# Kernel tuning notes

Measured on AMD Instinct MI355X. Metric: run time of the kernel, lower is better.

The kernel has to match this reference:

```python
import jax, jax.numpy as jnp
import numpy as np


def setup_inputs() -> dict:
    key = jax.random.key(0)
    k1, k2, k3 = jax.random.split(key, 3)
    B, H, D, N = 2, 16, 64, 2048
    return {
        "query": jax.random.normal(k1, (B, H, D, N), dtype=jnp.float32),
        "key": jax.random.normal(k2, (B, H, D, N), dtype=jnp.float32),
        "value": jax.random.normal(k3, (B, H, D, N), dtype=jnp.float32),
    }


def reference(query, key, value):
    # NOTE: original torch code scales by sqrt(query.size(-1)) which,
    # given the [B,H,d,N] layout, is sqrt(N) (the sequence length), not sqrt(d).
    scale = query.shape[-1] ** 0.5
    # scores[b,h,q,k] = sum_d query[b,h,d,q] * key[b,h,d,k]
    scores = jnp.einsum("bhdq,bhdk->bhqk", query, key) / scale
    attn = jax.nn.softmax(scores, axis=-1)
    # out[b,h,q,v] = sum_k attn[b,h,q,k] * value[b,h,v,k]
    return jnp.einsum("bhqk,bhvk->bhqv", attn, value)
```

## Files before the change

### kernel.cpp

```cpp
#include <hip/hip_runtime.h>
#include <hip/hip_bf16.h>


typedef __attribute__((ext_vector_type(8))) short short8;
typedef __attribute__((ext_vector_type(4))) float f32x4;

#define NN 2048
#define DD 64
#define ROWB 144

#if __has_builtin(__builtin_amdgcn_exp2f)
#define EXP2(x) __builtin_amdgcn_exp2f(x)
#else
#define EXP2(x) __expf(0.69314718056f * (x))
#endif

__device__ __forceinline__ unsigned pk2(float a, float b) {
  __hip_bfloat162 h = __float22bfloat162_rn(make_float2(a, b));
  unsigned u; __builtin_memcpy(&u, &h, 4); return u;
}
__device__ __forceinline__ short f2bf(float f) {
  union { float f; unsigned u; } x; x.f = f;
  unsigned r = (x.u + 0x7fffu + ((x.u >> 16) & 1u)) >> 16;
  return (short)r;
}

__global__ __launch_bounds__(256, 2) void attn_kernel(
    const float* __restrict__ Q, const float* __restrict__ K,
    const float* __restrict__ V, float* __restrict__ Out) {
  const int tid  = threadIdx.x;
  const int wave = tid >> 6, lane = tid & 63;
  const int quad = lane >> 4, l16 = lane & 15;

  const int bh   = blockIdx.x >> 4;
  const int qblk = blockIdx.x & 15;

  const float* Qh = Q + (size_t)bh * DD * NN;
  const float* Kh = K + (size_t)bh * DD * NN;
  const float* Vh = V + (size_t)bh * DD * NN;
  float*       Oh = Out + (size_t)bh * NN * DD;

  __shared__ __align__(16) char ldsK[2][64 * ROWB];
  __shared__ __align__(16) char ldsV[2][64 * ROWB];
  __shared__ __align__(16) char ldsP[8][16 * ROWB];

  const float qscale = 0.031881407f;
  short8 bQ[2][2];
  int qb[2];
#pragma unroll
  for (int qt = 0; qt < 2; ++qt) {
    qb[qt] = qblk * 128 + (wave * 2 + qt) * 16;
#pragma unroll
    for (int h = 0; h < 2; ++h)
#pragma unroll
      for (int j = 0; j < 8; ++j) {
        int d = h * 32 + quad * 8 + j;
        bQ[qt][h][j] = f2bf(Qh[(size_t)d * NN + qb[qt] + l16] * qscale);
      }
  }

  f32x4 accO[2][4];
#pragma unroll
  for (int qt = 0; qt < 2; ++qt)
#pragma unroll
    for (int vt = 0; vt < 4; ++vt) accO[qt][vt] = (f32x4){0.f, 0.f, 0.f, 0.f};
  float lp[2] = {0.f, 0.f};

  const int ka = tid & 31, kg = tid >> 5;
  const int vv = tid >> 2, vko = (tid & 3) * 16;
  const float* kbase0 = Kh + (size_t)(2 * ka) * NN + kg * 8;
  const float* kbase1 = kbase0 + NN;
  const float* vbase  = Vh + (size_t)vv * NN + vko;
  char* Pq0 = ldsP[wave * 2];
  char* Pq1 = ldsP[wave * 2 + 1];
  const int swr = l16 >> 1;

  float kA[8], kB[8], vA[16];
  auto load_kv = [&](int k0) {
    const float4* p0 = (const float4*)(kbase0 + k0);
    const float4* p1 = (const float4*)(kbase1 + k0);
    float4 a0 = p0[0], a1 = p0[1];
    float4 b0 = p1[0], b1 = p1[1];
    kA[0] = a0.x; kA[1] = a0.y; kA[2] = a0.z; kA[3] = a0.w;
    kA[4] = a1.x; kA[5] = a1.y; kA[6] = a1.z; kA[7] = a1.w;
    kB[0] = b0.x; kB[1] = b0.y; kB[2] = b0.z; kB[3] = b0.w;
    kB[4] = b1.x; kB[5] = b1.y; kB[6] = b1.z; kB[7] = b1.w;
    const float4* pv = (const float4*)(vbase + k0);
    float4 c0 = pv[0], c1 = pv[1], c2 = pv[2], c3 = pv[3];
    vA[0]  = c0.x; vA[1]  = c0.y; vA[2]  = c0.z; vA[3]  = c0.w;
    vA[4]  = c1.x; vA[5]  = c1.y; vA[6]  = c1.z; vA[7]  = c1.w;
    vA[8]  = c2.x; vA[9]  = c2.y; vA[10] = c2.z; vA[11] = c2.w;
    vA[12] = c3.x; vA[13] = c3.y; vA[14] = c3.z; vA[15] = c3.w;
  };
  auto store_kv = [&](char* bK, char* bV) {
#pragma unroll
    for (int j = 0; j < 8; ++j) {
      int k = kg * 8 + j;
      int grp = (ka >> 2) ^ ((k >> 1) & 7);
      *(unsigned*)&bK[k * ROWB + grp * 16 + (ka & 3) * 4] = pk2(kA[j], kB[j]);
    }
    uint4 w0 = make_uint4(pk2(vA[0], vA[1]),  pk2(vA[2], vA[3]),
                          pk2(vA[4], vA[5]),  pk2(vA[6], vA[7]));
    uint4 w1 = make_uint4(pk2(vA[8], vA[9]),  pk2(vA[10], vA[11]),
                          pk2(vA[12], vA[13]), pk2(vA[14], vA[15]));
    *(uint4*)&bV[vv * ROWB + vko * 2]      = w0;
    *(uint4*)&bV[vv * ROWB + vko * 2 + 16] = w1;
  };

  load_kv(0);
  store_kv(ldsK[0], ldsV[0]);
  __syncthreads();

  for (int it = 0; it < 32; ++it) {
    const int cur = it & 1;
    load_kv(((it + 1) & 31) * 64);

    const char* cK = ldsK[cur];
    const char* cV = ldsV[cur];

    f32x4 s[2][4];
#pragma unroll
    for (int kt = 0; kt < 4; ++kt) {
      const int key = kt * 16 + l16;
      short8 aK0 = *(const short8*)&cK[key * ROWB + ((quad) ^ swr) * 16];
      short8 aK1 = *(const short8*)&cK[key * ROWB + ((4 + quad) ^ swr) * 16];
      f32x4 z = (f32x4){0.f, 0.f, 0.f, 0.f};
      s[0][kt] = __builtin_amdgcn_mfma_f32_16x16x32_bf16(aK0, bQ[0][0], z, 0, 0, 0);
      s[0][kt] = __builtin_amdgcn_mfma_f32_16x16x32_bf16(aK1, bQ[0][1], s[0][kt], 0, 0, 0);
      s[1][kt] = __builtin_amdgcn_mfma_f32_16x16x32_bf16(aK0, bQ[1][0], z, 0, 0, 0);
      s[1][kt] = __builtin_amdgcn_mfma_f32_16x16x32_bf16(aK1, bQ[1][1], s[1][kt], 0, 0, 0);
    }

#pragma unroll
    for (int qt = 0; qt < 2; ++qt) {
      char* Pq = qt ? Pq1 : Pq0;
#pragma unroll
      for (int kt = 0; kt < 4; ++kt) {
        float p0 = EXP2(s[qt][kt][0]);
        float p1 = EXP2(s[qt][kt][1]);
        float p2 = EXP2(s[qt][kt][2]);
        float p3 = EXP2(s[qt][kt][3]);
        lp[qt] += (p0 + p1) + (p2 + p3);
        uint2 w; w.x = pk2(p0, p1); w.y = pk2(p2, p3);
        *(uint2*)&Pq[l16 * ROWB + kt * 32 + quad * 8] = w;
      }
    }

#pragma unroll
    for (int h2 = 0; h2 < 2; ++h2) {
      short8 aP0 = *(const short8*)&Pq0[l16 * ROWB + h2 * 64 + quad * 16];
      short8 aP1 = *(const short8*)&Pq1[l16 * ROWB + h2 * 64 + quad * 16];
#pragma unroll
      for (int vt = 0; vt < 4; ++vt) {
        short8 bV = *(const short8*)&cV[(vt * 16 + l16) * ROWB + h2 * 64 + quad * 16];
        accO[0][vt] = __builtin_amdgcn_mfma_f32_16x16x32_bf16(aP0, bV, accO[0][vt], 0, 0, 0);
        accO[1][vt] = __builtin_amdgcn_mfma_f32_16x16x32_bf16(aP1, bV, accO[1][vt], 0, 0, 0);
      }
    }

    store_kv(ldsK[cur ^ 1], ldsV[cur ^ 1]);
    __syncthreads();
  }

#pragma unroll
  for (int qt = 0; qt < 2; ++qt) {
    float l = lp[qt];
    l += __shfl_xor(l, 16, 64);
    l += __shfl_xor(l, 32, 64);
#pragma unroll
    for (int r = 0; r < 4; ++r) {
      float lr  = __shfl(l, quad * 4 + r, 64);
      float inv = 1.0f / lr;
      int q = qb[qt] + quad * 4 + r;
#pragma unroll
      for (int vt = 0; vt < 4; ++vt)
        Oh[(size_t)q * DD + vt * 16 + l16] = accO[qt][vt][r] * inv;
    }
  }
}

extern "C" void kernel_launch(void* const* d_in, const int* in_sizes, int n_in,
                              void* d_out, int out_size, void* d_ws, size_t ws_size,
                              hipStream_t stream) {
  const float* Q = (const float*)d_in[0];
  const float* K = (const float*)d_in[1];
  const float* V = (const float*)d_in[2];
  float* O = (float*)d_out;
  dim3 grid(2 * 16 * (NN / 128));
  attn_kernel<<<grid, dim3(256), 0, stream>>>(Q, K, V, O);
}
```

Baseline: 139.3 us.

## Switch to 32x32x16 MFMA and keep P in registers via permlane32 swap

Replaces the 16x16x32 MFMA tiling with 32x32x16 MFMAs, so each wave computes a 32-query by 64-key score tile as S^T. The exponentiated P values are packed to bf16 and rearranged across lane halves with v_permlane32_swap instead of being written to and re-read from a per-wave LDS buffer. This removes the P LDS round trip and its shared memory, and lowers instruction count per FLOP. In exchange it uses larger accumulator register sets, which may pressure occupancy, and relies on a gfx950-specific instruction.

```diff
diff --git a/kernel.cpp b/kernel.cpp
--- a/kernel.cpp
+++ b/kernel.cpp
@@ -3,7 +3,7 @@
 
 
 typedef __attribute__((ext_vector_type(8))) short short8;
-typedef __attribute__((ext_vector_type(4))) float f32x4;
+typedef __attribute__((ext_vector_type(16))) float f32x16;
 
 #define NN 2048
 #define DD 64
@@ -16,13 +16,16 @@
 #endif
 
 __device__ __forceinline__ unsigned pk2(float a, float b) {
-  __hip_bfloat162 h = __float22bfloat162_rn(make_float2(a, b));
-  unsigned u; __builtin_memcpy(&u, &h, 4); return u;
+  __hip_bfloat162 hh = __float22bfloat162_rn(make_float2(a, b));
+  unsigned u; __builtin_memcpy(&u, &hh, 4); return u;
 }
 __device__ __forceinline__ short f2bf(float f) {
   union { float f; unsigned u; } x; x.f = f;
   unsigned r = (x.u + 0x7fffu + ((x.u >> 16) & 1u)) >> 16;
   return (short)r;
+}
+__device__ __forceinline__ void pl32swap(unsigned &x, unsigned &y) {
+  asm("v_permlane32_swap_b32 %0, %1" : "+v"(x), "+v"(y));
 }
 
 __global__ __launch_bounds__(256, 2) void attn_kernel(
@@ -30,7 +33,7 @@
     const float* __restrict__ V, float* __restrict__ Out) {
   const int tid  = threadIdx.x;
   const int wave = tid >> 6, lane = tid & 63;
-  const int quad = lane >> 4, l16 = lane & 15;
+  const int m = lane & 31, h = lane >> 5;
 
   const int bh   = blockIdx.x >> 4;
   const int qblk = blockIdx.x & 15;
@@ -42,38 +45,30 @@
 
   __shared__ __align__(16) char ldsK[2][64 * ROWB];
   __shared__ __align__(16) char ldsV[2][64 * ROWB];
-  __shared__ __align__(16) char ldsP[8][16 * ROWB];
 
   const float qscale = 0.031881407f;
-  short8 bQ[2][2];
-  int qb[2];
+  const int qb = qblk * 128 + wave * 32;
+  short8 bQ[4];
 #pragma unroll
-  for (int qt = 0; qt < 2; ++qt) {
-    qb[qt] = qblk * 128 + (wave * 2 + qt) * 16;
+  for (int st = 0; st < 4; ++st)
 #pragma unroll
-    for (int h = 0; h < 2; ++h)
+    for (int j = 0; j < 8; ++j) {
+      int d = st * 16 + h * 8 + j;
+      bQ[st][j] = f2bf(Qh[(size_t)d * NN + qb + m] * qscale);
+    }
+
+  f32x16 accO[2];
 #pragma unroll
-      for (int j = 0; j < 8; ++j) {
-        int d = h * 32 + quad * 8 + j;
-        bQ[qt][h][j] = f2bf(Qh[(size_t)d * NN + qb[qt] + l16] * qscale);
-      }
-  }
-
-  f32x4 accO[2][4];
+  for (int vt = 0; vt < 2; ++vt)
 #pragma unroll
-  for (int qt = 0; qt < 2; ++qt)
-#pragma unroll
-    for (int vt = 0; vt < 4; ++vt) accO[qt][vt] = (f32x4){0.f, 0.f, 0.f, 0.f};
-  float lp[2] = {0.f, 0.f};
+    for (int i = 0; i < 16; ++i) accO[vt][i] = 0.f;
+  float lp = 0.f;
 
   const int ka = tid & 31, kg = tid >> 5;
   const int vv = tid >> 2, vko = (tid & 3) * 16;
   const float* kbase0 = Kh + (size_t)(2 * ka) * NN + kg * 8;
   const float* kbase1 = kbase0 + NN;
   const float* vbase  = Vh + (size_t)vv * NN + vko;
-  char* Pq0 = ldsP[wave * 2];
-  char* Pq1 = ldsP[wave * 2 + 1];
-  const int swr = l16 >> 1;
 
   float kA[8], kB[8], vA[16];
   auto load_kv = [&](int k0) {
@@ -111,6 +106,8 @@
   store_kv(ldsK[0], ldsV[0]);
   __syncthreads();
 
+  const int sw = (m >> 1) & 7;
+
   for (int it = 0; it < 32; ++it) {
     const int cur = it & 1;
     load_kv(((it + 1) & 31) * 64);
@@ -118,43 +115,50 @@
     const char* cK = ldsK[cur];
     const char* cV = ldsV[cur];
 
-    f32x4 s[2][4];
+    f32x16 sT0, sT1;
 #pragma unroll
-    for (int kt = 0; kt < 4; ++kt) {
-      const int key = kt * 16 + l16;
-      short8 aK0 = *(const short8*)&cK[key * ROWB + ((quad) ^ swr) * 16];
-      short8 aK1 = *(const short8*)&cK[key * ROWB + ((4 + quad) ^ swr) * 16];
-      f32x4 z = (f32x4){0.f, 0.f, 0.f, 0.f};
-      s[0][kt] = __builtin_amdgcn_mfma_f32_16x16x32_bf16(aK0, bQ[0][0], z, 0, 0, 0);
-      s[0][kt] = __builtin_amdgcn_mfma_f32_16x16x32_bf16(aK1, bQ[0][1], s[0][kt], 0, 0, 0);
-      s[1][kt] = __builtin_amdgcn_mfma_f32_16x16x32_bf16(aK0, bQ[1][0], z, 0, 0, 0);
-      s[1][kt] = __builtin_amdgcn_mfma_f32_16x16x32_bf16(aK1, bQ[1][1], s[1][kt], 0, 0, 0);
+    for (int i = 0; i < 16; ++i) { sT0[i] = 0.f; sT1[i] = 0.f; }
+#pragma unroll
+    for (int st = 0; st < 4; ++st) {
+      const int off = (((st * 2 + h) ^ sw) * 16);
+      short8 aK0 = *(const short8*)&cK[m * ROWB + off];
+      short8 aK1 = *(const short8*)&cK[(32 + m) * ROWB + off];
+      sT0 = __builtin_amdgcn_mfma_f32_32x32x16_bf16(aK0, bQ[st], sT0, 0, 0, 0);
+      sT1 = __builtin_amdgcn_mfma_f32_32x32x16_bf16(aK1, bQ[st], sT1, 0, 0, 0);
+    }
+
+    float p[2][16];
+#pragma unroll
+    for (int r = 0; r < 16; ++r) { p[0][r] = EXP2(sT0[r]); p[1][r] = EXP2(sT1[r]); }
+
+    unsigned u[2][4][2];
+#pragma unroll
+    for (int kt = 0; kt < 2; ++kt) {
+#pragma unroll
+      for (int g = 0; g < 4; ++g) {
+        u[kt][g][0] = pk2(p[kt][4 * g + 0], p[kt][4 * g + 1]);
+        u[kt][g][1] = pk2(p[kt][4 * g + 2], p[kt][4 * g + 3]);
+      }
+      float s0 = (p[kt][0]  + p[kt][1])  + (p[kt][2]  + p[kt][3]);
+      float s1 = (p[kt][4]  + p[kt][5])  + (p[kt][6]  + p[kt][7]);
+      float s2 = (p[kt][8]  + p[kt][9])  + (p[kt][10] + p[kt][11]);
+      float s3 = (p[kt][12] + p[kt][13]) + (p[kt][14] + p[kt][15]);
+      lp += (s0 + s1) + (s2 + s3);
     }
 
 #pragma unroll
-    for (int qt = 0; qt < 2; ++qt) {
-      char* Pq = qt ? Pq1 : Pq0;
+    for (int s = 0; s < 4; ++s) {
+      const int kt = s >> 1, ge = 2 * (s & 1);
+      unsigned t0 = u[kt][ge][0], t1 = u[kt][ge][1];
+      unsigned t2 = u[kt][ge + 1][0], t3 = u[kt][ge + 1][1];
+      pl32swap(t0, t2);
+      pl32swap(t1, t3);
+      short8 aP;
+      { unsigned w[4] = {t0, t1, t2, t3}; __builtin_memcpy(&aP, w, 16); }
 #pragma unroll
-      for (int kt = 0; kt < 4; ++kt) {
-        float p0 = EXP2(s[qt][kt][0]);
-        float p1 = EXP2(s[qt][kt][1]);
-        float p2 = EXP2(s[qt][kt][2]);
-        float p3 = EXP2(s[qt][kt][3]);
-        lp[qt] += (p0 + p1) + (p2 + p3);
-        uint2 w; w.x = pk2(p0, p1); w.y = pk2(p2, p3);
-        *(uint2*)&Pq[l16 * ROWB + kt * 32 + quad * 8] = w;
-      }
-    }
-
-#pragma unroll
-    for (int h2 = 0; h2 < 2; ++h2) {
-      short8 aP0 = *(const short8*)&Pq0[l16 * ROWB + h2 * 64 + quad * 16];
-      short8 aP1 = *(const short8*)&Pq1[l16 * ROWB + h2 * 64 + quad * 16];
-#pragma unroll
-      for (int vt = 0; vt < 4; ++vt) {
-        short8 bV = *(const short8*)&cV[(vt * 16 + l16) * ROWB + h2 * 64 + quad * 16];
-        accO[0][vt] = __builtin_amdgcn_mfma_f32_16x16x32_bf16(aP0, bV, accO[0][vt], 0, 0, 0);
-        accO[1][vt] = __builtin_amdgcn_mfma_f32_16x16x32_bf16(aP1, bV, accO[1][vt], 0, 0, 0);
+      for (int vt = 0; vt < 2; ++vt) {
+        short8 bV = *(const short8*)&cV[(vt * 32 + m) * ROWB + s * 32 + h * 16];
+        accO[vt] = __builtin_amdgcn_mfma_f32_32x32x16_bf16(aP, bV, accO[vt], 0, 0, 0);
       }
     }
 
@@ -162,20 +166,14 @@
     __syncthreads();
   }
 
+  float lv = lp + __shfl_xor(lp, 32, 64);
 #pragma unroll
-  for (int qt = 0; qt < 2; ++qt) {
-    float l = lp[qt];
-    l += __shfl_xor(l, 16, 64);
-    l += __shfl_xor(l, 32, 64);
-#pragma unroll
-    for (int r = 0; r < 4; ++r) {
-      float lr  = __shfl(l, quad * 4 + r, 64);
-      float inv = 1.0f / lr;
-      int q = qb[qt] + quad * 4 + r;
-#pragma unroll
-      for (int vt = 0; vt < 4; ++vt)
-        Oh[(size_t)q * DD + vt * 16 + l16] = accO[qt][vt][r] * inv;
-    }
+  for (int r = 0; r < 16; ++r) {
+    const int qrow = (r & 3) + 8 * (r >> 2) + 4 * h;
+    const float linv = 1.0f / __shfl(lv, qrow, 64);
+    float* op = Oh + (size_t)(qb + qrow) * DD + m;
+    op[0]  = accO[0][r] * linv;
+    op[32] = accO[1][r] * linv;
   }
 }
 
```

Result: slower. 145.1 us (+4.1%).

## Keep P in registers via permlane swaps and use 8 waves per block

Applied to the files above, without the earlier changes.

The per-wave P staging buffer in LDS is removed. The exp'd scores are repacked from the MFMA output layout into the A-operand layout with v_permlane32/16_swap, so the PV MFMA reads P straight from registers. The block grows to 512 threads, each wave owning one 16-query tile instead of two, which halves per-wave accumulators and spreads the K/V global loads over more threads. This trades LDS round trips and half the waves' work for more waves and more barrier participants per block, and depends on the swap permutation matching the operand layout.

```diff
diff --git a/kernel.cpp b/kernel.cpp
--- a/kernel.cpp
+++ b/kernel.cpp
@@ -16,16 +16,22 @@
 #endif
 
 __device__ __forceinline__ unsigned pk2(float a, float b) {
-  __hip_bfloat162 h = __float22bfloat162_rn(make_float2(a, b));
-  unsigned u; __builtin_memcpy(&u, &h, 4); return u;
+  __hip_bfloat162 hh = __float22bfloat162_rn(make_float2(a, b));
+  unsigned u; __builtin_memcpy(&u, &hh, 4); return u;
 }
 __device__ __forceinline__ short f2bf(float f) {
   union { float f; unsigned u; } x; x.f = f;
   unsigned r = (x.u + 0x7fffu + ((x.u >> 16) & 1u)) >> 16;
   return (short)r;
 }
+__device__ __forceinline__ void pl32swap(unsigned &x, unsigned &y) {
+  asm("v_permlane32_swap_b32 %0, %1" : "+v"(x), "+v"(y));
+}
+__device__ __forceinline__ void pl16swap(unsigned &x, unsigned &y) {
+  asm("v_permlane16_swap_b32 %0, %1" : "+v"(x), "+v"(y));
+}
 
-__global__ __launch_bounds__(256, 2) void attn_kernel(
+__global__ __launch_bounds__(512, 4) void attn_kernel(
     const float* __restrict__ Q, const float* __restrict__ K,
     const float* __restrict__ V, float* __restrict__ Out) {
   const int tid  = threadIdx.x;
@@ -42,74 +48,57 @@
 
   __shared__ __align__(16) char ldsK[2][64 * ROWB];
   __shared__ __align__(16) char ldsV[2][64 * ROWB];
-  __shared__ __align__(16) char ldsP[8][16 * ROWB];
 
   const float qscale = 0.031881407f;
-  short8 bQ[2][2];
-  int qb[2];
+  const int qb = qblk * 128 + wave * 16;
+  short8 bQ[2];
 #pragma unroll
-  for (int qt = 0; qt < 2; ++qt) {
-    qb[qt] = qblk * 128 + (wave * 2 + qt) * 16;
+  for (int hh = 0; hh < 2; ++hh)
 #pragma unroll
-    for (int h = 0; h < 2; ++h)
+    for (int j = 0; j < 8; ++j) {
+      int d = hh * 32 + quad * 8 + j;
+      bQ[hh][j] = f2bf(Qh[(size_t)d * NN + qb + l16] * qscale);
+    }
+
+  f32x4 accO[4];
 #pragma unroll
-      for (int j = 0; j < 8; ++j) {
-        int d = h * 32 + quad * 8 + j;
-        bQ[qt][h][j] = f2bf(Qh[(size_t)d * NN + qb[qt] + l16] * qscale);
-      }
-  }
-
-  f32x4 accO[2][4];
-#pragma unroll
-  for (int qt = 0; qt < 2; ++qt)
-#pragma unroll
-    for (int vt = 0; vt < 4; ++vt) accO[qt][vt] = (f32x4){0.f, 0.f, 0.f, 0.f};
-  float lp[2] = {0.f, 0.f};
+  for (int vt = 0; vt < 4; ++vt) accO[vt] = (f32x4){0.f, 0.f, 0.f, 0.f};
+  float lp = 0.f;
 
   const int ka = tid & 31, kg = tid >> 5;
-  const int vv = tid >> 2, vko = (tid & 3) * 16;
-  const float* kbase0 = Kh + (size_t)(2 * ka) * NN + kg * 8;
+  const int vv = tid >> 3, vko = (tid & 7) * 8;
+  const float* kbase0 = Kh + (size_t)(2 * ka) * NN + kg * 4;
   const float* kbase1 = kbase0 + NN;
   const float* vbase  = Vh + (size_t)vv * NN + vko;
-  char* Pq0 = ldsP[wave * 2];
-  char* Pq1 = ldsP[wave * 2 + 1];
-  const int swr = l16 >> 1;
 
-  float kA[8], kB[8], vA[16];
+  float kA[4], kB[4], vA[8];
   auto load_kv = [&](int k0) {
-    const float4* p0 = (const float4*)(kbase0 + k0);
-    const float4* p1 = (const float4*)(kbase1 + k0);
-    float4 a0 = p0[0], a1 = p0[1];
-    float4 b0 = p1[0], b1 = p1[1];
-    kA[0] = a0.x; kA[1] = a0.y; kA[2] = a0.z; kA[3] = a0.w;
-    kA[4] = a1.x; kA[5] = a1.y; kA[6] = a1.z; kA[7] = a1.w;
-    kB[0] = b0.x; kB[1] = b0.y; kB[2] = b0.z; kB[3] = b0.w;
-    kB[4] = b1.x; kB[5] = b1.y; kB[6] = b1.z; kB[7] = b1.w;
+    float4 a = *(const float4*)(kbase0 + k0);
+    float4 b = *(const float4*)(kbase1 + k0);
+    kA[0] = a.x; kA[1] = a.y; kA[2] = a.z; kA[3] = a.w;
+    kB[0] = b.x; kB[1] = b.y; kB[2] = b.z; kB[3] = b.w;
     const float4* pv = (const float4*)(vbase + k0);
-    float4 c0 = pv[0], c1 = pv[1], c2 = pv[2], c3 = pv[3];
-    vA[0]  = c0.x; vA[1]  = c0.y; vA[2]  = c0.z; vA[3]  = c0.w;
-    vA[4]  = c1.x; vA[5]  = c1.y; vA[6]  = c1.z; vA[7]  = c1.w;
-    vA[8]  = c2.x; vA[9]  = c2.y; vA[10] = c2.z; vA[11] = c2.w;
-    vA[12] = c3.x; vA[13] = c3.y; vA[14] = c3.z; vA[15] = c3.w;
+    float4 c0 = pv[0], c1 = pv[1];
+    vA[0] = c0.x; vA[1] = c0.y; vA[2] = c0.z; vA[3] = c0.w;
+    vA[4] = c1.x; vA[5] = c1.y; vA[6] = c1.z; vA[7] = c1.w;
   };
   auto store_kv = [&](char* bK, char* bV) {
 #pragma unroll
-    for (int j = 0; j < 8; ++j) {
-      int k = kg * 8 + j;
+    for (int j = 0; j < 4; ++j) {
+      int k = kg * 4 + j;
       int grp = (ka >> 2) ^ ((k >> 1) & 7);
       *(unsigned*)&bK[k * ROWB + grp * 16 + (ka & 3) * 4] = pk2(kA[j], kB[j]);
     }
-    uint4 w0 = make_uint4(pk2(vA[0], vA[1]),  pk2(vA[2], vA[3]),
-                          pk2(vA[4], vA[5]),  pk2(vA[6], vA[7]));
-    uint4 w1 = make_uint4(pk2(vA[8], vA[9]),  pk2(vA[10], vA[11]),
-                          pk2(vA[12], vA[13]), pk2(vA[14], vA[15]));
-    *(uint4*)&bV[vv * ROWB + vko * 2]      = w0;
-    *(uint4*)&bV[vv * ROWB + vko * 2 + 16] = w1;
+    uint4 w = make_uint4(pk2(vA[0], vA[1]), pk2(vA[2], vA[3]),
+                         pk2(vA[4], vA[5]), pk2(vA[6], vA[7]));
+    *(uint4*)&bV[vv * ROWB + vko * 2] = w;
   };
 
   load_kv(0);
   store_kv(ldsK[0], ldsV[0]);
   __syncthreads();
+
+  const int swr = l16 >> 1;
 
   for (int it = 0; it < 32; ++it) {
     const int cur = it & 1;
@@ -118,43 +107,34 @@
     const char* cK = ldsK[cur];
     const char* cV = ldsV[cur];
 
-    f32x4 s[2][4];
+    unsigned u[4][2];
 #pragma unroll
     for (int kt = 0; kt < 4; ++kt) {
-      const int key = kt * 16 + l16;
-      short8 aK0 = *(const short8*)&cK[key * ROWB + ((quad) ^ swr) * 16];
-      short8 aK1 = *(const short8*)&cK[key * ROWB + ((4 + quad) ^ swr) * 16];
+      const char* row = &cK[(kt * 16 + l16) * ROWB];
+      short8 aK0 = *(const short8*)&row[(quad ^ swr) * 16];
+      short8 aK1 = *(const short8*)&row[((4 + quad) ^ swr) * 16];
       f32x4 z = (f32x4){0.f, 0.f, 0.f, 0.f};
-      s[0][kt] = __builtin_amdgcn_mfma_f32_16x16x32_bf16(aK0, bQ[0][0], z, 0, 0, 0);
-      s[0][kt] = __builtin_amdgcn_mfma_f32_16x16x32_bf16(aK1, bQ[0][1], s[0][kt], 0, 0, 0);
-      s[1][kt] = __builtin_amdgcn_mfma_f32_16x16x32_bf16(aK0, bQ[1][0], z, 0, 0, 0);
-      s[1][kt] = __builtin_amdgcn_mfma_f32_16x16x32_bf16(aK1, bQ[1][1], s[1][kt], 0, 0, 0);
+      f32x4 sT = __builtin_amdgcn_mfma_f32_16x16x32_bf16(aK0, bQ[0], z, 0, 0, 0);
+      sT = __builtin_amdgcn_mfma_f32_16x16x32_bf16(aK1, bQ[1], sT, 0, 0, 0);
+      float p0 = EXP2(sT[0]), p1 = EXP2(sT[1]);
+      float p2 = EXP2(sT[2]), p3 = EXP2(sT[3]);
+      lp += (p0 + p1) + (p2 + p3);
+      u[kt][0] = pk2(p0, p1);
+      u[kt][1] = pk2(p2, p3);
     }
 
 #pragma unroll
-    for (int qt = 0; qt < 2; ++qt) {
-      char* Pq = qt ? Pq1 : Pq0;
-#pragma unroll
-      for (int kt = 0; kt < 4; ++kt) {
-        float p0 = EXP2(s[qt][kt][0]);
-        float p1 = EXP2(s[qt][kt][1]);
-        float p2 = EXP2(s[qt][kt][2]);
-        float p3 = EXP2(s[qt][kt][3]);
-        lp[qt] += (p0 + p1) + (p2 + p3);
-        uint2 w; w.x = pk2(p0, p1); w.y = pk2(p2, p3);
-        *(uint2*)&Pq[l16 * ROWB + kt * 32 + quad * 8] = w;
-      }
-    }
-
-#pragma unroll
-    for (int h2 = 0; h2 < 2; ++h2) {
-      short8 aP0 = *(const short8*)&Pq0[l16 * ROWB + h2 * 64 + quad * 16];
-      short8 aP1 = *(const short8*)&Pq1[l16 * ROWB + h2 * 64 + quad * 16];
+    for (int ks = 0; ks < 2; ++ks) {
+      unsigned c0 = u[2 * ks][0], c2 = u[2 * ks + 1][0];
+      pl32swap(c0, c2); pl16swap(c0, c2);
+      unsigned c1 = u[2 * ks][1], c3 = u[2 * ks + 1][1];
+      pl32swap(c1, c3); pl16swap(c1, c3);
+      short8 aP;
+      { unsigned w[4] = {c0, c1, c2, c3}; __builtin_memcpy(&aP, w, 16); }
 #pragma unroll
       for (int vt = 0; vt < 4; ++vt) {
-        short8 bV = *(const short8*)&cV[(vt * 16 + l16) * ROWB + h2 * 64 + quad * 16];
-        accO[0][vt] = __builtin_amdgcn_mfma_f32_16x16x32_bf16(aP0, bV, accO[0][vt], 0, 0, 0);
-        accO[1][vt] = __builtin_amdgcn_mfma_f32_16x16x32_bf16(aP1, bV, accO[1][vt], 0, 0, 0);
+        short8 bVf = *(const short8*)&cV[(vt * 16 + l16) * ROWB + ks * 64 + quad * 16];
+        accO[vt] = __builtin_amdgcn_mfma_f32_16x16x32_bf16(aP, bVf, accO[vt], 0, 0, 0);
       }
     }
 
@@ -162,20 +142,17 @@
     __syncthreads();
   }
 
+  float lv = lp;
+  lv += __shfl_xor(lv, 16, 64);
+  lv += __shfl_xor(lv, 32, 64);
 #pragma unroll
-  for (int qt = 0; qt < 2; ++qt) {
-    float l = lp[qt];
-    l += __shfl_xor(l, 16, 64);
-    l += __shfl_xor(l, 32, 64);
+  for (int r = 0; r < 4; ++r) {
+    float lr  = __shfl(lv, quad * 4 + r, 64);
+    float inv = 1.0f / lr;
+    int q = qb + quad * 4 + r;
 #pragma unroll
-    for (int r = 0; r < 4; ++r) {
-      float lr  = __shfl(l, quad * 4 + r, 64);
-      float inv = 1.0f / lr;
-      int q = qb[qt] + quad * 4 + r;
-#pragma unroll
-      for (int vt = 0; vt < 4; ++vt)
-        Oh[(size_t)q * DD + vt * 16 + l16] = accO[qt][vt][r] * inv;
-    }
+    for (int vt = 0; vt < 4; ++vt)
+      Oh[(size_t)q * DD + vt * 16 + l16] = accO[vt][r] * inv;
   }
 }
 
@@ -187,5 +164,5 @@
   const float* V = (const float*)d_in[2];
   float* O = (float*)d_out;
   dim3 grid(2 * 16 * (NN / 128));
-  attn_kernel<<<grid, dim3(256), 0, stream>>>(Q, K, V, O);
+  attn_kernel<<<grid, dim3(512), 0, stream>>>(Q, K, V, O);
 }
```

Result: slower. 142.6 us (+2.3%).

## Split key range across two wave groups and pass P through registers via permlane

Applied to the files above, without the earlier changes.

The block grows to 512 threads in two 4-wave groups. Each group processes half of the key sequence for the same 128 queries, with its own double-buffered K/V tiles, and the partial outputs and row sums are merged through LDS at the end. The P matrix is no longer written to and read back from LDS: it is rearranged in registers with v_permlane32/16_swap, and the S, exp and PV steps are interleaved per 32-key slice. This aims to double the parallelism per query block and remove LDS traffic for P, at the cost of a final reduction step and higher register and LDS pressure per block.

```diff
diff --git a/kernel.cpp b/kernel.cpp
--- a/kernel.cpp
+++ b/kernel.cpp
@@ -8,6 +8,9 @@
 #define NN 2048
 #define DD 64
 #define ROWB 144
+#define KHALF 1024
+#define CMB_STRIDE 65
+#define LBASE 8320
 
 #if __has_builtin(__builtin_amdgcn_exp2f)
 #define EXP2(x) __builtin_amdgcn_exp2f(x)
@@ -16,21 +19,29 @@
 #endif
 
 __device__ __forceinline__ unsigned pk2(float a, float b) {
-  __hip_bfloat162 h = __float22bfloat162_rn(make_float2(a, b));
-  unsigned u; __builtin_memcpy(&u, &h, 4); return u;
+  __hip_bfloat162 hh = __float22bfloat162_rn(make_float2(a, b));
+  unsigned u; __builtin_memcpy(&u, &hh, 4); return u;
 }
 __device__ __forceinline__ short f2bf(float f) {
   union { float f; unsigned u; } x; x.f = f;
   unsigned r = (x.u + 0x7fffu + ((x.u >> 16) & 1u)) >> 16;
   return (short)r;
 }
-
-__global__ __launch_bounds__(256, 2) void attn_kernel(
+__device__ __forceinline__ void pl32swap(unsigned &x, unsigned &y) {
+  asm("v_permlane32_swap_b32 %0, %1" : "+v"(x), "+v"(y));
+}
+__device__ __forceinline__ void pl16swap(unsigned &x, unsigned &y) {
+  asm("v_permlane16_swap_b32 %0, %1" : "+v"(x), "+v"(y));
+}
+
+__global__ __launch_bounds__(512, 4) void attn_kernel(
     const float* __restrict__ Q, const float* __restrict__ K,
     const float* __restrict__ V, float* __restrict__ Out) {
   const int tid  = threadIdx.x;
   const int wave = tid >> 6, lane = tid & 63;
   const int quad = lane >> 4, l16 = lane & 15;
+  const int grp  = wave >> 2;
+  const int w4   = wave & 3;
 
   const int bh   = blockIdx.x >> 4;
   const int qblk = blockIdx.x & 15;
@@ -40,24 +51,20 @@
   const float* Vh = V + (size_t)bh * DD * NN;
   float*       Oh = Out + (size_t)bh * NN * DD;
 
-  __shared__ __align__(16) char ldsK[2][64 * ROWB];
-  __shared__ __align__(16) char ldsV[2][64 * ROWB];
-  __shared__ __align__(16) char ldsP[8][16 * ROWB];
+  __shared__ __align__(16) char ldsKV[2][2][2][64 * ROWB];
 
   const float qscale = 0.031881407f;
+  const int qb = qblk * 128 + w4 * 32;
   short8 bQ[2][2];
-  int qb[2];
-#pragma unroll
-  for (int qt = 0; qt < 2; ++qt) {
-    qb[qt] = qblk * 128 + (wave * 2 + qt) * 16;
-#pragma unroll
-    for (int h = 0; h < 2; ++h)
+#pragma unroll
+  for (int qt = 0; qt < 2; ++qt)
+#pragma unroll
+    for (int hh = 0; hh < 2; ++hh)
 #pragma unroll
       for (int j = 0; j < 8; ++j) {
-        int d = h * 32 + quad * 8 + j;
-        bQ[qt][h][j] = f2bf(Qh[(size_t)d * NN + qb[qt] + l16] * qscale);
-      }
-  }
+        int d = hh * 32 + quad * 8 + j;
+        bQ[qt][hh][j] = f2bf(Qh[(size_t)d * NN + qb + qt * 16 + l16] * qscale);
+      }
 
   f32x4 accO[2][4];
 #pragma unroll
@@ -66,14 +73,13 @@
     for (int vt = 0; vt < 4; ++vt) accO[qt][vt] = (f32x4){0.f, 0.f, 0.f, 0.f};
   float lp[2] = {0.f, 0.f};
 
-  const int ka = tid & 31, kg = tid >> 5;
-  const int vv = tid >> 2, vko = (tid & 3) * 16;
-  const float* kbase0 = Kh + (size_t)(2 * ka) * NN + kg * 8;
+  const int t  = tid & 255;
+  const int ka = t & 31, kg = t >> 5;
+  const int vv = t >> 2, vko = (t & 3) * 16;
+  const int kb = grp * KHALF;
+  const float* kbase0 = Kh + (size_t)(2 * ka) * NN + kb + kg * 8;
   const float* kbase1 = kbase0 + NN;
-  const float* vbase  = Vh + (size_t)vv * NN + vko;
-  char* Pq0 = ldsP[wave * 2];
-  char* Pq1 = ldsP[wave * 2 + 1];
-  const int swr = l16 >> 1;
+  const float* vbase  = Vh + (size_t)vv * NN + kb + vko;
 
   float kA[8], kB[8], vA[16];
   auto load_kv = [&](int k0) {
@@ -96,8 +102,8 @@
 #pragma unroll
     for (int j = 0; j < 8; ++j) {
       int k = kg * 8 + j;
-      int grp = (ka >> 2) ^ ((k >> 1) & 7);
-      *(unsigned*)&bK[k * ROWB + grp * 16 + (ka & 3) * 4] = pk2(kA[j], kB[j]);
+      int g = (ka >> 2) ^ ((k >> 1) & 7);
+      *(unsigned*)&bK[k * ROWB + g * 16 + (ka & 3) * 4] = pk2(kA[j], kB[j]);
     }
     uint4 w0 = make_uint4(pk2(vA[0], vA[1]),  pk2(vA[2], vA[3]),
                           pk2(vA[4], vA[5]),  pk2(vA[6], vA[7]));
@@ -108,73 +114,98 @@
   };
 
   load_kv(0);
-  store_kv(ldsK[0], ldsV[0]);
+  store_kv(&ldsKV[grp][0][0][0], &ldsKV[grp][0][1][0]);
   __syncthreads();
 
-  for (int it = 0; it < 32; ++it) {
+  const int swr = l16 >> 1;
+
+  for (int it = 0; it < 16; ++it) {
     const int cur = it & 1;
-    load_kv(((it + 1) & 31) * 64);
-
-    const char* cK = ldsK[cur];
-    const char* cV = ldsV[cur];
-
-    f32x4 s[2][4];
-#pragma unroll
-    for (int kt = 0; kt < 4; ++kt) {
-      const int key = kt * 16 + l16;
-      short8 aK0 = *(const short8*)&cK[key * ROWB + ((quad) ^ swr) * 16];
-      short8 aK1 = *(const short8*)&cK[key * ROWB + ((4 + quad) ^ swr) * 16];
-      f32x4 z = (f32x4){0.f, 0.f, 0.f, 0.f};
-      s[0][kt] = __builtin_amdgcn_mfma_f32_16x16x32_bf16(aK0, bQ[0][0], z, 0, 0, 0);
-      s[0][kt] = __builtin_amdgcn_mfma_f32_16x16x32_bf16(aK1, bQ[0][1], s[0][kt], 0, 0, 0);
-      s[1][kt] = __builtin_amdgcn_mfma_f32_16x16x32_bf16(aK0, bQ[1][0], z, 0, 0, 0);
-      s[1][kt] = __builtin_amdgcn_mfma_f32_16x16x32_bf16(aK1, bQ[1][1], s[1][kt], 0, 0, 0);
+    load_kv(((it + 1) & 15) * 64);
+
+    const char* cK = &ldsKV[grp][cur][0][0];
+    const char* cV = &ldsKV[grp][cur][1][0];
+
+#pragma unroll
+    for (int ks = 0; ks < 2; ++ks) {
+      unsigned u[2][2][2];
+#pragma unroll
+      for (int k2 = 0; k2 < 2; ++k2) {
+        const int kt = ks * 2 + k2;
+        const char* row = &cK[(kt * 16 + l16) * ROWB];
+        short8 aK0 = *(const short8*)&row[(quad ^ swr) * 16];
+        short8 aK1 = *(const short8*)&row[((4 + quad) ^ swr) * 16];
+#pragma unroll
+        for (int qt = 0; qt < 2; ++qt) {
+          f32x4 z = (f32x4){0.f, 0.f, 0.f, 0.f};
+          f32x4 sT = __builtin_amdgcn_mfma_f32_16x16x32_bf16(aK0, bQ[qt][0], z, 0, 0, 0);
+          sT = __builtin_amdgcn_mfma_f32_16x16x32_bf16(aK1, bQ[qt][1], sT, 0, 0, 0);
+          float p0 = EXP2(sT[0]), p1 = EXP2(sT[1]);
+          float p2 = EXP2(sT[2]), p3 = EXP2(sT[3]);
+          lp[qt] += (p0 + p1) + (p2 + p3);
+          u[qt][k2][0] = pk2(p0, p1);
+          u[qt][k2][1] = pk2(p2, p3);
+        }
+      }
+      short8 aP[2];
+#pragma unroll
+      for (int qt = 0; qt < 2; ++qt) {
+        unsigned c0 = u[qt][0][0], c2 = u[qt][1][0];
+        pl32swap(c0, c2); pl16swap(c0, c2);
+        unsigned c1 = u[qt][0][1], c3 = u[qt][1][1];
+        pl32swap(c1, c3); pl16swap(c1, c3);
+        unsigned w[4] = {c0, c1, c2, c3};
+        __builtin_memcpy(&aP[qt], w, 16);
+      }
+#pragma unroll
+      for (int vt = 0; vt < 4; ++vt) {
+        short8 bVf = *(const short8*)&cV[(vt * 16 + l16) * ROWB + ks * 64 + quad * 16];
+        accO[0][vt] = __builtin_amdgcn_mfma_f32_16x16x32_bf16(aP[0], bVf, accO[0][vt], 0, 0, 0);
+        accO[1][vt] = __builtin_amdgcn_mfma_f32_16x16x32_bf16(aP[1], bVf, accO[1][vt], 0, 0, 0);
+      }
     }
 
-#pragma unroll
-    for (int qt = 0; qt < 2; ++qt) {
-      char* Pq = qt ? Pq1 : Pq0;
-#pragma unroll
-      for (int kt = 0; kt < 4; ++kt) {
-        float p0 = EXP2(s[qt][kt][0]);
-        float p1 = EXP2(s[qt][kt][1]);
-        float p2 = EXP2(s[qt][kt][2]);
-        float p3 = EXP2(s[qt][kt][3]);
-        lp[qt] += (p0 + p1) + (p2 + p3);
-        uint2 w; w.x = pk2(p0, p1); w.y = pk2(p2, p3);
-        *(uint2*)&Pq[l16 * ROWB + kt * 32 + quad * 8] = w;
-      }
-    }
-
-#pragma unroll
-    for (int h2 = 0; h2 < 2; ++h2) {
-      short8 aP0 = *(const short8*)&Pq0[l16 * ROWB + h2 * 64 + quad * 16];
-      short8 aP1 = *(const short8*)&Pq1[l16 * ROWB + h2 * 64 + quad * 16];
-#pragma unroll
-      for (int vt = 0; vt < 4; ++vt) {
-        short8 bV = *(const short8*)&cV[(vt * 16 + l16) * ROWB + h2 * 64 + quad * 16];
-        accO[0][vt] = __builtin_amdgcn_mfma_f32_16x16x32_bf16(aP0, bV, accO[0][vt], 0, 0, 0);
-        accO[1][vt] = __builtin_amdgcn_mfma_f32_16x16x32_bf16(aP1, bV, accO[1][vt], 0, 0, 0);
-      }
-    }
-
-    store_kv(ldsK[cur ^ 1], ldsV[cur ^ 1]);
+    store_kv(&ldsKV[grp][cur ^ 1][0][0], &ldsKV[grp][cur ^ 1][1][0]);
     __syncthreads();
   }
 
+  float lv[2];
 #pragma unroll
   for (int qt = 0; qt < 2; ++qt) {
-    float l = lp[qt];
-    l += __shfl_xor(l, 16, 64);
-    l += __shfl_xor(l, 32, 64);
+    float x = lp[qt];
+    x += __shfl_xor(x, 16, 64);
+    x += __shfl_xor(x, 32, 64);
+    lv[qt] = x;
+  }
+
+  float* cmb = (float*)&ldsKV[0][0][0][0];
+  const int giveq = 1 - grp;
+  {
+    float* rg = cmb + (w4 * 2 + giveq) * (16 * CMB_STRIDE);
+#pragma unroll
+    for (int vt = 0; vt < 4; ++vt)
+#pragma unroll
+      for (int r = 0; r < 4; ++r)
+        rg[(quad * 4 + r) * CMB_STRIDE + vt * 16 + l16] = accO[giveq][vt][r];
+    if (lane < 16) cmb[LBASE + (w4 * 2 + giveq) * 16 + l16] = lv[giveq];
+  }
+  __syncthreads();
+  {
+    float* rk = cmb + (w4 * 2 + grp) * (16 * CMB_STRIDE);
+#pragma unroll
+    for (int vt = 0; vt < 4; ++vt)
+#pragma unroll
+      for (int r = 0; r < 4; ++r)
+        accO[grp][vt][r] += rk[(quad * 4 + r) * CMB_STRIDE + vt * 16 + l16];
+    float lfull = lv[grp] + cmb[LBASE + (w4 * 2 + grp) * 16 + l16];
 #pragma unroll
     for (int r = 0; r < 4; ++r) {
-      float lr  = __shfl(l, quad * 4 + r, 64);
+      float lr  = __shfl(lfull, quad * 4 + r, 64);
       float inv = 1.0f / lr;
-      int q = qb[qt] + quad * 4 + r;
+      int q = qb + grp * 16 + quad * 4 + r;
 #pragma unroll
       for (int vt = 0; vt < 4; ++vt)
-        Oh[(size_t)q * DD + vt * 16 + l16] = accO[qt][vt][r] * inv;
+        Oh[(size_t)q * DD + vt * 16 + l16] = accO[grp][vt][r] * inv;
     }
   }
 }
@@ -187,5 +218,5 @@
   const float* V = (const float*)d_in[2];
   float* O = (float*)d_out;
   dim3 grid(2 * 16 * (NN / 128));
-  attn_kernel<<<grid, dim3(256), 0, stream>>>(Q, K, V, O);
-}
+  attn_kernel<<<grid, dim3(512), 0, stream>>>(Q, K, V, O);
+}
```

Measured after the change: 176.8 us. 26.9% more time.
